# Kernel tuning notes

Hardware: AMD Instinct MI355X
Metric: run time of the kernel (lower is better)

Reference implementation:

```python
import jax, jax.numpy as jnp
import numpy as np

HEAD_NUM = 16
KEY_DIM = 64
EMBED = 1024
KV_OUT = HEAD_NUM * KEY_DIM  # 1024


def setup_inputs() -> dict:
    key = jax.random.key(0)
    ks = jax.random.split(key, 11)
    B, L, E = 2, 2048, EMBED
    scale = 0.02
    return {
        "query": jax.random.normal(ks[0], (B, L, E), jnp.float32),
        "key": jax.random.normal(ks[1], (B, L, E), jnp.float32),
        "value": jax.random.normal(ks[2], (B, L, E), jnp.float32),
        "W_Query": jax.random.normal(ks[3], (E, KV_OUT), jnp.float32) * scale,
        "W_Key": jax.random.normal(ks[4], (E, KV_OUT), jnp.float32) * scale,
        "W_Value": jax.random.normal(ks[5], (E, KV_OUT), jnp.float32) * scale,
        "W_Output": jax.random.normal(ks[6], (KV_OUT, E), jnp.float32) * scale,
        "B_Query": jnp.zeros((KV_OUT,), jnp.float32),
        "B_Key": jnp.zeros((KV_OUT,), jnp.float32),
        "B_Value": jnp.zeros((KV_OUT,), jnp.float32),
        "B_Output": jnp.zeros((E,), jnp.float32),
    }


def reference(query, key, value, W_Query, W_Key, W_Value, W_Output,
              B_Query, B_Key, B_Value, B_Output):
    B, Lq, E = query.shape
    Lk = key.shape[1]
    H, D = HEAD_NUM, KEY_DIM
    # QKV projections + bias
    q = query @ W_Query + B_Query            # [B, Lq, H*D]
    k = key @ W_Key + B_Key                  # [B, Lk, H*D]
    v = value @ W_Value + B_Value            # [B, Lk, H*D]
    # tf.split(axis=2) per head == reshape to [B, L, H, D]
    q = q.reshape(B, Lq, H, D)
    k = k.reshape(B, Lk, H, D)
    v = v.reshape(B, Lk, H, D)
    # scaled dot-product attention (no mask, dropout=0)
    scores = jnp.einsum("bqhd,bkhd->bhqk", q, k) / (D ** 0.5)
    probs = jax.nn.softmax(scores, axis=-1)
    out = jnp.einsum("bhqk,bkhd->bqhd", probs, v)  # [B, Lq, H, D]
    out = out.reshape(B, Lq, H * D)
    return out @ W_Output + B_Output
```

## Files before the change

kernel.cpp:

```cpp
#include <hip/hip_runtime.h>

using u16 = unsigned short;
using u32 = unsigned int;

typedef __attribute__((ext_vector_type(8))) short bf16x8;
typedef __attribute__((ext_vector_type(4))) float f32x4;
typedef __attribute__((ext_vector_type(4))) u32 u32x4;
typedef __attribute__((ext_vector_type(2))) u32 u32x2;
typedef __attribute__((ext_vector_type(4))) _Float16 f16x4;

#define MFMA_BF16_K32(a, b, c) __builtin_amdgcn_mfma_f32_16x16x32_bf16((a), (b), (c), 0, 0, 0)
#define MFMA_F16_K16(a, b, c) __builtin_amdgcn_mfma_f32_16x16x16f16((a), (b), (c), 0, 0, 0)

#define QSCALE 0.18033688011112042f

extern "C" __device__ float __ocml_native_exp2_f32(float);

__device__ __forceinline__ u16 f2bf(float f) {
  u32 u = __builtin_bit_cast(u32, f);
  return (u16)((u + 0x7fffu + ((u >> 16) & 1u)) >> 16);
}

__device__ __forceinline__ u32 pk_f16(float a, float b) {
  auto v = __builtin_amdgcn_cvt_pkrtz(a, b);
  return __builtin_bit_cast(u32, v);
}

__device__ __forceinline__ void load_lds16(const void* g, void* l) {
  __builtin_amdgcn_global_load_lds((__attribute__((address_space(1))) void*)g,
                                   (__attribute__((address_space(3))) void*)l,
                                   16, 0, 0);
}

__global__ __launch_bounds__(256) void cvt_all_kernel(
    const float* __restrict__ q, const float* __restrict__ k, const float* __restrict__ v,
    u16* __restrict__ oq, u16* __restrict__ ok, u16* __restrict__ ov,
    const float* __restrict__ w0, const float* __restrict__ w1,
    const float* __restrict__ w2, const float* __restrict__ w3,
    u16* __restrict__ d0, u16* __restrict__ d1,
    u16* __restrict__ d2, u16* __restrict__ d3) {
  const int id = blockIdx.x;
  const int tid = threadIdx.x;
  if (id < 6144) {
    const int z = id >> 11, bx = id & 2047;
    const float* s = z == 0 ? q : z == 1 ? k : v;
    u16* d = z == 0 ? oq : z == 1 ? ok : ov;
    int i = (bx * 256 + tid) * 8;
    f32x4 a = *(const f32x4*)(s + i);
    f32x4 b = *(const f32x4*)(s + i + 4);
    u32x4 o;
    o.x = (u32)f2bf(a.x) | ((u32)f2bf(a.y) << 16);
    o.y = (u32)f2bf(a.z) | ((u32)f2bf(a.w) << 16);
    o.z = (u32)f2bf(b.x) | ((u32)f2bf(b.y) << 16);
    o.w = (u32)f2bf(b.z) | ((u32)f2bf(b.w) << 16);
    *(u32x4*)(d + i) = o;
    return;
  }
  __shared__ float t[64][65];
  const int r0 = id - 6144;
  const int z = r0 >> 8, rr0 = r0 & 255;
  const int bx = rr0 & 15, by = rr0 >> 4;
  const float* src = z == 0 ? w0 : z == 1 ? w1 : z == 2 ? w2 : w3;
  u16* dst = z == 0 ? d0 : z == 1 ? d1 : z == 2 ? d2 : d3;
  const float scale = (z == 0) ? QSCALE : 1.0f;
  const int r = tid >> 4, c4 = (tid & 15) * 4;
#pragma unroll
  for (int i = 0; i < 4; ++i) {
    int row = r + i * 16;
    f32x4 vv = *(const f32x4*)(src + (by * 64 + row) * 1024 + bx * 64 + c4);
    t[row][c4 + 0] = vv.x;
    t[row][c4 + 1] = vv.y;
    t[row][c4 + 2] = vv.z;
    t[row][c4 + 3] = vv.w;
  }
  __syncthreads();
  const int rw = tid >> 2, cc = (tid & 3) * 16;
  alignas(16) u16 tmp[16];
#pragma unroll
  for (int j = 0; j < 16; ++j) tmp[j] = f2bf(t[cc + j][rw] * scale);
  u32x4* outp = (u32x4*)(dst + (bx * 64 + rw) * 1024 + by * 64 + cc);
  outp[0] = *(const u32x4*)&tmp[0];
  outp[1] = *(const u32x4*)&tmp[8];
}

__global__ __launch_bounds__(256) void gemm_qkv_kernel(
    const u16* __restrict__ x0, const u16* __restrict__ x1, const u16* __restrict__ x2,
    const u16* __restrict__ w0, const u16* __restrict__ w1, const u16* __restrict__ w2,
    const float* __restrict__ b0, const float* __restrict__ b1, const float* __restrict__ b2,
    u16* __restrict__ c0, u16* __restrict__ c1, u16* __restrict__ vt) {
  __shared__ u16 As[128 * 64];
  __shared__ u16 Bs[128 * 64];
  const int lid = blockIdx.x;
  const int xcd = lid & 7, rr = lid >> 3;
  const int nb = rr & 7, slot = rr >> 3;
  const int g = slot * 8 + xcd;
  const int z = g >> 5, m_idx = g & 31;
  const u16* A = z == 0 ? x0 : z == 1 ? x1 : x2;
  const u16* Bt = z == 0 ? w0 : z == 1 ? w1 : w2;
  const float* bias = z == 0 ? b0 : z == 1 ? b1 : b2;
  const float bscale = z == 0 ? QSCALE : 1.0f;
  const int tid = threadIdx.x;
  const int wave = tid >> 6, lane = tid & 63;
  const int l16 = lane & 15, quad = lane >> 4;
  const int l7 = l16 & 7;
  const int wm = wave >> 1, wn = wave & 1;
  const int m0 = m_idx * 128, n0 = nb * 128;

  f32x4 acc[4][4];
  const f32x4 zf = {0.f, 0.f, 0.f, 0.f};
#pragma unroll
  for (int i = 0; i < 4; ++i)
#pragma unroll
    for (int j = 0; j < 4; ++j) acc[i][j] = zf;

  for (int kb = 0; kb < 1024; kb += 64) {
#pragma unroll
    for (int t = 0; t < 4; ++t) {
      int c = wave * 256 + t * 64 + lane;
      int row = c >> 3, sc8 = (c & 7) ^ (row & 7);
      load_lds16(A + (m0 + row) * 1024 + kb + sc8 * 8, &As[(wave * 256 + t * 64) * 8]);
    }
#pragma unroll
    for (int t = 0; t < 4; ++t) {
      int c = wave * 256 + t * 64 + lane;
      int row = c >> 3, sc8 = (c & 7) ^ (row & 7);
      load_lds16(Bt + (n0 + row) * 1024 + kb + sc8 * 8, &Bs[(wave * 256 + t * 64) * 8]);
    }
    asm volatile("s_waitcnt vmcnt(0)" ::: "memory");
    __syncthreads();
#pragma unroll
    for (int ks = 0; ks < 2; ++ks) {
      const int sch = (ks * 4 + quad) ^ l7;
      bf16x8 af[4], bfv[4];
#pragma unroll
      for (int mt = 0; mt < 4; ++mt)
        af[mt] = *(const bf16x8*)&As[(wm * 64 + mt * 16 + l16) * 64 + sch * 8];
#pragma unroll
      for (int nt = 0; nt < 4; ++nt)
        bfv[nt] = *(const bf16x8*)&Bs[(wn * 64 + nt * 16 + l16) * 64 + sch * 8];
#pragma unroll
      for (int mt = 0; mt < 4; ++mt)
#pragma unroll
        for (int nt = 0; nt < 4; ++nt) acc[mt][nt] = MFMA_BF16_K32(af[mt], bfv[nt], acc[mt][nt]);
    }
    __syncthreads();
  }

  float bv[4];
#pragma unroll
  for (int nt = 0; nt < 4; ++nt) bv[nt] = bias[n0 + wn * 64 + nt * 16 + l16] * bscale;
  if (z != 2) {
    u16* C = z == 0 ? c0 : c1;
#pragma unroll
    for (int mt = 0; mt < 4; ++mt)
#pragma unroll
      for (int nt = 0; nt < 4; ++nt)
#pragma unroll
        for (int r = 0; r < 4; ++r) {
          int row = m0 + wm * 64 + mt * 16 + quad * 4 + r;
          int col = n0 + wn * 64 + nt * 16 + l16;
          C[row * 1024 + col] = f2bf(acc[mt][nt][r] + bv[nt]);
        }
  } else {
#pragma unroll
    for (int mt = 0; mt < 4; ++mt)
#pragma unroll
      for (int nt = 0; nt < 4; ++nt)
#pragma unroll
        for (int r = 0; r < 4; ++r) {
          int row = m0 + wm * 64 + mt * 16 + quad * 4 + r;
          int col = n0 + wn * 64 + nt * 16 + l16;
          int bb = row >> 11, kv = row & 2047;
          _Float16 hv = (_Float16)(acc[mt][nt][r] + bv[nt]);
          vt[(bb * 1024 + col) * 2048 + kv] = __builtin_bit_cast(u16, hv);
        }
  }
}

__global__ __launch_bounds__(256) void gemm_out_kernel(const u16* __restrict__ A,
                                                       const u16* __restrict__ Bt,
                                                       const float* __restrict__ bias,
                                                       float* __restrict__ C) {
  __shared__ u16 As[64 * 64];
  __shared__ u16 Bs[128 * 64];
  const int lid = blockIdx.x;
  const int xcd = lid & 7, rr = lid >> 3;
  const int nb = rr & 7, slot = rr >> 3;
  const int by = slot * 8 + xcd;
  const int tid = threadIdx.x;
  const int wave = tid >> 6, lane = tid & 63;
  const int l16 = lane & 15, quad = lane >> 4;
  const int l7 = l16 & 7;
  const int m0 = by * 64, n0 = nb * 128;

  f32x4 acc[4][2];
  const f32x4 zf = {0.f, 0.f, 0.f, 0.f};
#pragma unroll
  for (int i = 0; i < 4; ++i)
#pragma unroll
    for (int j = 0; j < 2; ++j) acc[i][j] = zf;

  for (int kb = 0; kb < 1024; kb += 64) {
#pragma unroll
    for (int t = 0; t < 2; ++t) {
      int c = wave * 128 + t * 64 + lane;
      int row = c >> 3, sc8 = (c & 7) ^ (row & 7);
      load_lds16(A + (m0 + row) * 1024 + kb + sc8 * 8, &As[(wave * 128 + t * 64) * 8]);
    }
#pragma unroll
    for (int t = 0; t < 4; ++t) {
      int c = wave * 256 + t * 64 + lane;
      int row = c >> 3, sc8 = (c & 7) ^ (row & 7);
      load_lds16(Bt + (n0 + row) * 1024 + kb + sc8 * 8, &Bs[(wave * 256 + t * 64) * 8]);
    }
    asm volatile("s_waitcnt vmcnt(0)" ::: "memory");
    __syncthreads();
#pragma unroll
    for (int ks = 0; ks < 2; ++ks) {
      const int sch = (ks * 4 + quad) ^ l7;
      bf16x8 af[4], bfv[2];
#pragma unroll
      for (int mt = 0; mt < 4; ++mt)
        af[mt] = *(const bf16x8*)&As[(mt * 16 + l16) * 64 + sch * 8];
#pragma unroll
      for (int nt = 0; nt < 2; ++nt)
        bfv[nt] = *(const bf16x8*)&Bs[(wave * 32 + nt * 16 + l16) * 64 + sch * 8];
#pragma unroll
      for (int mt = 0; mt < 4; ++mt)
#pragma unroll
        for (int nt = 0; nt < 2; ++nt) acc[mt][nt] = MFMA_BF16_K32(af[mt], bfv[nt], acc[mt][nt]);
    }
    __syncthreads();
  }

  float bv[2];
#pragma unroll
  for (int nt = 0; nt < 2; ++nt) bv[nt] = bias[n0 + wave * 32 + nt * 16 + l16];
#pragma unroll
  for (int mt = 0; mt < 4; ++mt)
#pragma unroll
    for (int nt = 0; nt < 2; ++nt)
#pragma unroll
      for (int r = 0; r < 4; ++r) {
        int row = m0 + mt * 16 + quad * 4 + r;
        int col = n0 + wave * 32 + nt * 16 + l16;
        C[row * 1024 + col] = acc[mt][nt][r] + bv[nt];
      }
}

__global__ __launch_bounds__(256) void flash_kernel(const u16* __restrict__ Q,
                                                    const u16* __restrict__ K,
                                                    const u16* __restrict__ Vt,
                                                    u16* __restrict__ O) {
  __shared__ float bufA[4096];
  __shared__ float bufB[4096];
  __shared__ float lred[4][64];
  __shared__ float lfin[64];
  const int tid = threadIdx.x;
  const int wave = tid >> 6, lane = tid & 63;
  const int l16 = lane & 15, quad = lane >> 4;
  const int l7 = l16 & 7;
  const int id = blockIdx.x;
  const int xcd = id & 7, slot = id >> 3;
  const int pair = xcd * 4 + (slot & 3);
  const int qb = slot >> 2;
  const int b = pair >> 4, h = pair & 15;
  const u16* Qh = Q + (b * 2048 + qb * 64) * 1024 + h * 64;
  const u16* Kh = K + b * 2048 * 1024 + h * 64;
  const u16* Vh = Vt + pair * 64 * 2048;

  u16* qlds = (u16*)bufA;
#pragma unroll
  for (int t = 0; t < 2; ++t) {
    int c = (t * 4 + wave) * 64 + lane;
    int row = c >> 3, sc8 = (c & 7) ^ (row & 7);
    load_lds16(Qh + row * 1024 + sc8 * 8, &qlds[((t * 4 + wave) * 64) * 8]);
  }
  asm volatile("s_waitcnt vmcnt(0)" ::: "memory");
  __syncthreads();
  bf16x8 qf[4][2];
#pragma unroll
  for (int qn = 0; qn < 4; ++qn)
#pragma unroll
    for (int ks = 0; ks < 2; ++ks)
      qf[qn][ks] = *(const bf16x8*)&qlds[(qn * 16 + l16) * 64 + (((ks * 4 + quad) ^ l7)) * 8];
  __syncthreads();

  f32x4 o_acc[4][4];
  const f32x4 zf = {0.f, 0.f, 0.f, 0.f};
#pragma unroll
  for (int qn = 0; qn < 4; ++qn)
#pragma unroll
    for (int dt = 0; dt < 4; ++dt) o_acc[qn][dt] = zf;
  float lp[4] = {0.f, 0.f, 0.f, 0.f};

  for (int kb = 0; kb < 16; ++kb) {
    const int kv0 = kb * 128;
    u32x4 kf[2][2];
    u32x2 vf[2][4];
#pragma unroll
    for (int c2 = 0; c2 < 2; ++c2) {
      const int kvrow = kv0 + (wave * 2 + c2) * 16 + l16;
#pragma unroll
      for (int ks = 0; ks < 2; ++ks)
        kf[c2][ks] = *(const u32x4*)(Kh + kvrow * 1024 + ks * 32 + quad * 8);
      const int kvc = kv0 + (wave * 2 + c2) * 16 + quad * 4;
#pragma unroll
      for (int dt = 0; dt < 4; ++dt)
        vf[c2][dt] = *(const u32x2*)(Vh + (dt * 16 + l16) * 2048 + kvc);
    }
#pragma unroll
    for (int c2 = 0; c2 < 2; ++c2) {
      f32x4 s_acc[4];
#pragma unroll
      for (int qn = 0; qn < 4; ++qn) s_acc[qn] = zf;
#pragma unroll
      for (int ks = 0; ks < 2; ++ks) {
        bf16x8 kfr = __builtin_bit_cast(bf16x8, kf[c2][ks]);
#pragma unroll
        for (int qn = 0; qn < 4; ++qn) s_acc[qn] = MFMA_BF16_K32(kfr, qf[qn][ks], s_acc[qn]);
      }
      union { u32 u[2]; f16x4 v; } pkv[4];
#pragma unroll
      for (int qn = 0; qn < 4; ++qn) {
        float e0 = __ocml_native_exp2_f32(s_acc[qn].x);
        float e1 = __ocml_native_exp2_f32(s_acc[qn].y);
        float e2 = __ocml_native_exp2_f32(s_acc[qn].z);
        float e3 = __ocml_native_exp2_f32(s_acc[qn].w);
        lp[qn] += (e0 + e1) + (e2 + e3);
        pkv[qn].u[0] = pk_f16(e0, e1);
        pkv[qn].u[1] = pk_f16(e2, e3);
      }
#pragma unroll
      for (int dt = 0; dt < 4; ++dt) {
        f16x4 vfr = __builtin_bit_cast(f16x4, vf[c2][dt]);
#pragma unroll
        for (int qn = 0; qn < 4; ++qn)
          o_acc[qn][dt] = MFMA_F16_K16(pkv[qn].v, vfr, o_acc[qn][dt]);
      }
    }
  }

#pragma unroll
  for (int qn = 0; qn < 4; ++qn) {
    lp[qn] += __shfl_xor(lp[qn], 16);
    lp[qn] += __shfl_xor(lp[qn], 32);
  }
  if (quad == 0) {
#pragma unroll
    for (int qn = 0; qn < 4; ++qn) lred[wave][qn * 16 + l16] = lp[qn];
  }
  if (wave == 1 || wave == 3) {
    float* buf = (wave == 1) ? bufA : bufB;
#pragma unroll
    for (int qm = 0; qm < 4; ++qm)
#pragma unroll
      for (int dt = 0; dt < 4; ++dt)
        *(f32x4*)&buf[(((qm * 4 + dt) * 4 + quad) * 16 + l16) * 4] = o_acc[qm][dt];
  }
  __syncthreads();
  if (tid < 64) lfin[tid] = lred[0][tid] + lred[1][tid] + lred[2][tid] + lred[3][tid];
  if (wave == 0 || wave == 2) {
    float* buf = (wave == 0) ? bufA : bufB;
#pragma unroll
    for (int qm = 0; qm < 4; ++qm)
#pragma unroll
      for (int dt = 0; dt < 4; ++dt)
        o_acc[qm][dt] += *(const f32x4*)&buf[(((qm * 4 + dt) * 4 + quad) * 16 + l16) * 4];
  }
  __syncthreads();
  if (wave == 2) {
#pragma unroll
    for (int qm = 0; qm < 4; ++qm)
#pragma unroll
      for (int dt = 0; dt < 4; ++dt)
        *(f32x4*)&bufA[(((qm * 4 + dt) * 4 + quad) * 16 + l16) * 4] = o_acc[qm][dt];
  }
  __syncthreads();
  if (wave == 0) {
#pragma unroll
    for (int qm = 0; qm < 4; ++qm)
#pragma unroll
      for (int dt = 0; dt < 4; ++dt)
        o_acc[qm][dt] += *(const f32x4*)&bufA[(((qm * 4 + dt) * 4 + quad) * 16 + l16) * 4];
#pragma unroll
    for (int qm = 0; qm < 4; ++qm)
#pragma unroll
      for (int r = 0; r < 4; ++r) {
        int qrow = qm * 16 + quad * 4 + r;
        float inv = 1.0f / lfin[qrow];
        int row = b * 2048 + qb * 64 + qrow;
#pragma unroll
        for (int dt = 0; dt < 4; ++dt)
          O[row * 1024 + h * 64 + dt * 16 + l16] = f2bf(o_acc[qm][dt][r] * inv);
      }
  }
}

extern "C" void kernel_launch(void* const* d_in, const int* in_sizes, int n_in,
                              void* d_out, int out_size, void* d_ws, size_t ws_size,
                              hipStream_t stream) {
  const float* q = (const float*)d_in[0];
  const float* k = (const float*)d_in[1];
  const float* v = (const float*)d_in[2];
  const float* Wq = (const float*)d_in[3];
  const float* Wk = (const float*)d_in[4];
  const float* Wv = (const float*)d_in[5];
  const float* Wo = (const float*)d_in[6];
  const float* Bq = (const float*)d_in[7];
  const float* Bk = (const float*)d_in[8];
  const float* Bv = (const float*)d_in[9];
  const float* Bo = (const float*)d_in[10];
  float* out = (float*)d_out;

  char* w = (char*)d_ws;
  const size_t MB = 1u << 20;
  u16* xq = (u16*)(w + 0 * MB);
  u16* xk = (u16*)(w + 8 * MB);
  u16* xv = (u16*)(w + 16 * MB);
  u16* wqt = (u16*)(w + 24 * MB);
  u16* wkt = (u16*)(w + 26 * MB);
  u16* wvt = (u16*)(w + 28 * MB);
  u16* wot = (u16*)(w + 30 * MB);
  u16* Qp = (u16*)(w + 32 * MB);
  u16* Kp = (u16*)(w + 40 * MB);
  u16* Vtr = (u16*)(w + 48 * MB);
  u16* At = (u16*)(w + 56 * MB);

  cvt_all_kernel<<<dim3(7168), 256, 0, stream>>>(q, k, v, xq, xk, xv,
                                                 Wq, Wk, Wv, Wo, wqt, wkt, wvt, wot);
  gemm_qkv_kernel<<<dim3(768), 256, 0, stream>>>(xq, xk, xv, wqt, wkt, wvt,
                                                 Bq, Bk, Bv, Qp, Kp, Vtr);
  flash_kernel<<<dim3(1024), 256, 0, stream>>>(Qp, Kp, Vtr, At);
  gemm_out_kernel<<<dim3(512), 256, 0, stream>>>(At, wot, Bo, out);
}
```

Baseline: 265.7 us.

## Double-buffer per-wave K/V tiles in LDS via async global-to-LDS loads

Replaces direct per-lane global loads of K and V fragments in the flash attention loop with per-wave double-buffered LDS staging using load_lds16. The next 128-row K/V block is prefetched while the current one is consumed, with swizzled LDS layouts to avoid bank conflicts. The epilogue reuses the staging buffers. The aim is to hide global memory latency behind the MFMA work. In exchange LDS use grows, which could lower occupancy, and vmcnt-based waiting without a barrier relies on each wave touching only its own buffers.

```diff
diff --git a/kernel.cpp b/kernel.cpp
--- a/kernel.cpp
+++ b/kernel.cpp
@@ -252,8 +252,7 @@
                                                     const u16* __restrict__ K,
                                                     const u16* __restrict__ Vt,
                                                     u16* __restrict__ O) {
-  __shared__ float bufA[4096];
-  __shared__ float bufB[4096];
+  __shared__ u16 stage[4][2][4096];
   __shared__ float lred[4][64];
   __shared__ float lfin[64];
   const int tid = threadIdx.x;
@@ -266,10 +265,10 @@
   const int qb = slot >> 2;
   const int b = pair >> 4, h = pair & 15;
   const u16* Qh = Q + (b * 2048 + qb * 64) * 1024 + h * 64;
-  const u16* Kh = K + b * 2048 * 1024 + h * 64;
-  const u16* Vh = Vt + pair * 64 * 2048;
-
-  u16* qlds = (u16*)bufA;
+  const u16* Kh = K + b * 2048 * 1024 + h * 64 + wave * 32 * 1024;
+  const u16* Vh = Vt + pair * 64 * 2048 + wave * 32;
+
+  u16* qlds = &stage[0][0][0];
 #pragma unroll
   for (int t = 0; t < 2; ++t) {
     int c = (t * 4 + wave) * 64 + lane;
@@ -286,6 +285,16 @@
       qf[qn][ks] = *(const bf16x8*)&qlds[(qn * 16 + l16) * 64 + (((ks * 4 + quad) ^ l7)) * 8];
   __syncthreads();
 
+  u16* kb0 = &stage[wave][0][0];
+  u16* vb0 = &stage[wave][0][2048];
+  u16* kb1 = &stage[wave][1][0];
+  u16* vb1 = &stage[wave][1][2048];
+
+  const int k_srow = lane >> 3;
+  const int k_sc8 = (lane & 7) ^ (lane >> 3);
+  const int v_sd = lane >> 2;
+  const int v_sg = (lane & 3) ^ ((lane >> 3) & 3);
+
   f32x4 o_acc[4][4];
   const f32x4 zf = {0.f, 0.f, 0.f, 0.f};
 #pragma unroll
@@ -294,31 +303,42 @@
     for (int dt = 0; dt < 4; ++dt) o_acc[qn][dt] = zf;
   float lp[4] = {0.f, 0.f, 0.f, 0.f};
 
+#pragma unroll
+  for (int t = 0; t < 4; ++t)
+    load_lds16(Kh + (t * 8 + k_srow) * 1024 + k_sc8 * 8, kb0 + t * 512);
+#pragma unroll
+  for (int t = 0; t < 4; ++t)
+    load_lds16(Vh + (t * 16 + v_sd) * 2048 + v_sg * 8, vb0 + t * 512);
+
   for (int kb = 0; kb < 16; ++kb) {
-    const int kv0 = kb * 128;
-    u32x4 kf[2][2];
-    u32x2 vf[2][4];
+    u16* kc = (kb & 1) ? kb1 : kb0;
+    u16* vc = (kb & 1) ? vb1 : vb0;
+    if (kb < 15) {
+      u16* kn = (kb & 1) ? kb0 : kb1;
+      u16* vn = (kb & 1) ? vb0 : vb1;
+      const int kv1 = (kb + 1) * 128;
+#pragma unroll
+      for (int t = 0; t < 4; ++t)
+        load_lds16(Kh + (kv1 + t * 8 + k_srow) * 1024 + k_sc8 * 8, kn + t * 512);
+#pragma unroll
+      for (int t = 0; t < 4; ++t)
+        load_lds16(Vh + (t * 16 + v_sd) * 2048 + kv1 + v_sg * 8, vn + t * 512);
+      asm volatile("s_waitcnt vmcnt(8)" ::: "memory");
+    } else {
+      asm volatile("s_waitcnt vmcnt(0)" ::: "memory");
+    }
+
 #pragma unroll
     for (int c2 = 0; c2 < 2; ++c2) {
-      const int kvrow = kv0 + (wave * 2 + c2) * 16 + l16;
-#pragma unroll
-      for (int ks = 0; ks < 2; ++ks)
-        kf[c2][ks] = *(const u32x4*)(Kh + kvrow * 1024 + ks * 32 + quad * 8);
-      const int kvc = kv0 + (wave * 2 + c2) * 16 + quad * 4;
-#pragma unroll
-      for (int dt = 0; dt < 4; ++dt)
-        vf[c2][dt] = *(const u32x2*)(Vh + (dt * 16 + l16) * 2048 + kvc);
-    }
-#pragma unroll
-    for (int c2 = 0; c2 < 2; ++c2) {
+      const int rr = c2 * 16 + l16;
       f32x4 s_acc[4];
 #pragma unroll
       for (int qn = 0; qn < 4; ++qn) s_acc[qn] = zf;
 #pragma unroll
       for (int ks = 0; ks < 2; ++ks) {
-        bf16x8 kfr = __builtin_bit_cast(bf16x8, kf[c2][ks]);
-#pragma unroll
-        for (int qn = 0; qn < 4; ++qn) s_acc[qn] = MFMA_BF16_K32(kfr, qf[qn][ks], s_acc[qn]);
+        bf16x8 kf = *(const bf16x8*)&kc[rr * 64 + ((ks * 4 + quad) ^ l7) * 8];
+#pragma unroll
+        for (int qn = 0; qn < 4; ++qn) s_acc[qn] = MFMA_BF16_K32(kf, qf[qn][ks], s_acc[qn]);
       }
       union { u32 u[2]; f16x4 v; } pkv[4];
 #pragma unroll
@@ -333,14 +353,20 @@
       }
 #pragma unroll
       for (int dt = 0; dt < 4; ++dt) {
-        f16x4 vfr = __builtin_bit_cast(f16x4, vf[c2][dt]);
+        const int d = dt * 16 + l16;
+        f16x4 vf = *(const f16x4*)&vc[d * 32 +
+                                      ((c2 * 2 + (quad >> 1)) ^ ((l16 >> 1) & 3)) * 8 +
+                                      (quad & 1) * 4];
 #pragma unroll
         for (int qn = 0; qn < 4; ++qn)
-          o_acc[qn][dt] = MFMA_F16_K16(pkv[qn].v, vfr, o_acc[qn][dt]);
+          o_acc[qn][dt] = MFMA_F16_K16(pkv[qn].v, vf, o_acc[qn][dt]);
       }
     }
   }
 
+  __syncthreads();
+  float* bufA = (float*)&stage[0][0][0];
+  float* bufB = (float*)&stage[2][0][0];
 #pragma unroll
   for (int qn = 0; qn < 4; ++qn) {
     lp[qn] += __shfl_xor(lp[qn], 16);
```

Result: faster. 229.8 us (-13.5%).
